# Kernel optimization log

Measured on AMD Instinct MI355X. Metric: run time of the kernel, lower is better.

## Reference

```python
import jax, jax.numpy as jnp
import numpy as np

N = 16384        # tokens (batch*seq)
D_MODEL = 4096
D_HALF = D_MODEL // 2
NUM_EXPERTS = 64
TOP_K = 4
SCALE = 2.0


def setup_inputs() -> dict:
    key = jax.random.key(0)
    k_u, k_ex, k_ey = jax.random.split(key, 3)
    u = jax.random.normal(k_u, (N, D_MODEL), dtype=jnp.float32)
    E_x = jax.random.normal(k_ex, (D_HALF, NUM_EXPERTS), dtype=jnp.float32) * 0.01
    E_y = jax.random.normal(k_ey, (D_HALF, NUM_EXPERTS), dtype=jnp.float32) * 0.01
    bias = jnp.zeros((NUM_EXPERTS,), dtype=jnp.float32)
    # torus-shape scalar parameters (torch init values)
    c = jnp.float32(2.0)
    d = jnp.float32(2.0)
    a1 = jnp.float32(4.0)
    b1 = jnp.float32(4.0)
    return {"u": u, "E_x": E_x, "E_y": E_y, "bias": bias,
            "c": c, "d": d, "a1": a1, "b1": b1, "top_k": TOP_K}


def reference(u, E_x, E_y, bias, c, d, a1, b1, top_k):
    d_half = E_x.shape[0]
    num_experts = E_x.shape[1]
    # dual small GEMM + tanh squash onto [-scale, scale]
    x = jnp.tanh(u[..., :d_half] @ E_x) * SCALE        # [N, E]
    y = jnp.tanh(u[..., d_half:] @ E_y) * SCALE        # [N, E]
    xa, ya = jnp.abs(x), jnp.abs(y)
    # 4CM torus: f(x,y) = (|x|^a1 + |y|^b1) * exp(-(|x|^c + |y|^d))
    scores = (xa ** a1 + ya ** b1) * jnp.exp(-(xa ** c + ya ** d)) + bias
    topk_s, topk_i = jax.lax.top_k(scores, top_k)       # [N, k]
    probs = jax.nn.softmax(scores, axis=-1)             # [N, E]
    aux_loss = jnp.sum(jnp.mean(probs, axis=0) ** 2) * num_experts
    return topk_i, topk_s, scores, aux_loss
```

## Files before the change

### kernel.cpp

```cpp
#include <hip/hip_runtime.h>
#include <math.h>

#define N_TOK 16384
#define DM    4096
#define DH    2048
#define NE    64
#define TBK   64
#define TOPK  4
#define KQ    1024
#define NSTEP 32

#define OFF_TI  0
#define OFF_TS  (N_TOK * TOPK)
#define OFF_SC  (N_TOK * TOPK * 2)
#define OFF_AUX (N_TOK * TOPK * 2 + N_TOK * NE)

typedef __attribute__((ext_vector_type(4)))  float  f32x4;
typedef __attribute__((ext_vector_type(16))) float  f32x16;
typedef __attribute__((ext_vector_type(8)))  __bf16 bf16x8;

#define BSPLIT_ELEMS (2 * 64 * 3 * 2 * 2 * 64 * 8)

__device__ __forceinline__ void split3(float a, __bf16& h, __bf16& m, __bf16& l) {
    h = (__bf16)a;
    float r = a - (float)h;
    m = (__bf16)r;
    float r2 = r - (float)m;
    l = (__bf16)r2;
}

__global__ __launch_bounds__(256) void prep_B(
    const float* __restrict__ Ex, const float* __restrict__ Ey,
    __bf16* __restrict__ Bws)
{
    const int t    = blockIdx.x * 256 + threadIdx.x;
    const int lane = t & 63;
    const int sk   = (t >> 6) & 1;
    const int et   = (t >> 7) & 1;
    const int ks   = (t >> 8) & 63;
    const int h    = (t >> 14) & 1;
    const float* E = h ? Ey : Ex;
    const int e  = et * 32 + (lane & 31);
    const int k0 = ks * 32 + sk * 16 + (lane >> 5) * 8;
    bf16x8 vh, vm, vl;
    #pragma unroll
    for (int j = 0; j < 8; ++j) {
        __bf16 hh, mm, ll;
        split3(E[(size_t)(k0 + j) * NE + e], hh, mm, ll);
        vh[j] = hh; vm[j] = mm; vl[j] = ll;
    }
    #pragma unroll
    for (int s = 0; s < 3; ++s) {
        size_t base = ((((((size_t)h * 64 + ks) * 3 + s) * 2 + et) * 2 + sk) * 64 + lane) * 8;
        *(bf16x8*)(Bws + base) = (s == 0) ? vh : (s == 1) ? vm : vl;
    }
}

__global__ __launch_bounds__(512, 2) void torus_mfma(
    const float* __restrict__ u, const __bf16* __restrict__ Bws,
    const float* __restrict__ bias,
    const float* __restrict__ cp, const float* __restrict__ dp,
    const float* __restrict__ a1p, const float* __restrict__ b1p,
    float* __restrict__ out, float* __restrict__ esum)
{
    __shared__ float pre[2][NE][68];
    __shared__ float stile[TBK][NE + 1];
    __shared__ float s_m[TBK], s_inv[TBK];

    const int tid  = threadIdx.x;
    const int t0   = blockIdx.x * TBK;
    const int lane = tid & 63;
    const int wv   = tid >> 6;
    const int h    = wv >> 2;
    const int kh   = (wv >> 1) & 1;
    const int th   = wv & 1;
    const int lr   = lane & 31;
    const int lkh  = lane >> 5;

    const float* ap = u + (size_t)(t0 + th * 32 + lr) * DM + h * DH + kh * KQ + lkh * 8;
    const __bf16* bp0 = Bws + ((size_t)h * 64 + kh * 32) * 6144 + lane * 8;

    f32x16 acc[2] = {};
    f32x4  rA[2][4];

    auto load_raw = [&](f32x4 (&r)[4], int s) {
        const float* p = ap + s * 32;
        r[0] = *(const f32x4*)(p);
        r[1] = *(const f32x4*)(p + 4);
        r[2] = *(const f32x4*)(p + 16);
        r[3] = *(const f32x4*)(p + 20);
    };

    auto step = [&](int s, f32x4 (&r)[4]) {
        const __bf16* bp = bp0 + (size_t)s * 6144;
        bf16x8 bh[2][2], bm[2][2], bl[2][2];
        #pragma unroll
        for (int et = 0; et < 2; ++et)
            #pragma unroll
            for (int sk = 0; sk < 2; ++sk) {
                bh[et][sk] = *(const bf16x8*)(bp + (0 * 4 + et * 2 + sk) * 512);
                bm[et][sk] = *(const bf16x8*)(bp + (1 * 4 + et * 2 + sk) * 512);
                bl[et][sk] = *(const bf16x8*)(bp + (2 * 4 + et * 2 + sk) * 512);
            }
        bf16x8 sh[2], sm[2], sl[2];
        #pragma unroll
        for (int sk = 0; sk < 2; ++sk)
            #pragma unroll
            for (int q = 0; q < 2; ++q)
                #pragma unroll
                for (int j = 0; j < 4; ++j) {
                    __bf16 hh, mm, ll;
                    split3(r[sk * 2 + q][j], hh, mm, ll);
                    sh[sk][q * 4 + j] = hh; sm[sk][q * 4 + j] = mm; sl[sk][q * 4 + j] = ll;
                }
        const int sp = (s + 2 < NSTEP) ? s + 2 : s;
        load_raw(r, sp);
        #pragma unroll
        for (int et = 0; et < 2; ++et)
            #pragma unroll
            for (int sk = 0; sk < 2; ++sk) {
                acc[et] = __builtin_amdgcn_mfma_f32_32x32x16_bf16(sh[sk], bh[et][sk], acc[et], 0, 0, 0);
                acc[et] = __builtin_amdgcn_mfma_f32_32x32x16_bf16(sm[sk], bh[et][sk], acc[et], 0, 0, 0);
                acc[et] = __builtin_amdgcn_mfma_f32_32x32x16_bf16(sl[sk], bh[et][sk], acc[et], 0, 0, 0);
            }
        #pragma unroll
        for (int et = 0; et < 2; ++et)
            #pragma unroll
            for (int sk = 0; sk < 2; ++sk) {
                acc[et] = __builtin_amdgcn_mfma_f32_32x32x16_bf16(sh[sk], bm[et][sk], acc[et], 0, 0, 0);
                acc[et] = __builtin_amdgcn_mfma_f32_32x32x16_bf16(sm[sk], bm[et][sk], acc[et], 0, 0, 0);
            }
        #pragma unroll
        for (int et = 0; et < 2; ++et)
            #pragma unroll
            for (int sk = 0; sk < 2; ++sk)
                acc[et] = __builtin_amdgcn_mfma_f32_32x32x16_bf16(sh[sk], bl[et][sk], acc[et], 0, 0, 0);
    };

    load_raw(rA[0], 0);
    load_raw(rA[1], 1);
    #pragma unroll 1
    for (int s = 0; s < NSTEP; s += 2) {
        step(s,     rA[0]);
        step(s + 1, rA[1]);
    }

    __syncthreads();
    if (kh == 0) {
        #pragma unroll
        for (int et = 0; et < 2; ++et)
            #pragma unroll
            for (int q = 0; q < 4; ++q) {
                int e  = et * 32 + lr;
                int tk = th * 32 + q * 8 + 4 * lkh;
                f32x4 v = { acc[et][q*4+0], acc[et][q*4+1], acc[et][q*4+2], acc[et][q*4+3] };
                *(f32x4*)&pre[h][e][tk] = v;
            }
    }
    __syncthreads();
    if (kh == 1) {
        #pragma unroll
        for (int et = 0; et < 2; ++et)
            #pragma unroll
            for (int q = 0; q < 4; ++q) {
                int e  = et * 32 + lr;
                int tk = th * 32 + q * 8 + 4 * lkh;
                f32x4 v = { acc[et][q*4+0], acc[et][q*4+1], acc[et][q*4+2], acc[et][q*4+3] };
                f32x4 o = *(f32x4*)&pre[h][e][tk];
                v += o;
                *(f32x4*)&pre[h][e][tk] = v;
            }
    }
    __syncthreads();

    {
        const float c_ = *cp, d_ = *dp, a1_ = *a1p, b1_ = *b1p;
        const int tk = tid & 63;
        const int e0 = (tid >> 6) * 8;
        #pragma unroll
        for (int i = 0; i < 8; ++i) {
            int e = e0 + i;
            float x = pre[0][e][tk];
            float y = pre[1][e][tk];
            x = tanhf(x) * 2.0f; y = tanhf(y) * 2.0f;
            float xa = fabsf(x), ya = fabsf(y);
            float sc = (powf(xa, a1_) + powf(ya, b1_)) *
                       expf(-(powf(xa, c_) + powf(ya, d_))) + bias[e];
            stile[tk][e] = sc;
        }
    }
    __syncthreads();

    if (tid < TBK) {
        const int t = tid;
        float bv[TOPK]; int bi[TOPK];
        #pragma unroll
        for (int p = 0; p < TOPK; ++p) {
            float best = -INFINITY; int besti = 0;
            for (int e = 0; e < NE; ++e) {
                float v = stile[t][e];
                bool taken = false;
                #pragma unroll
                for (int q = 0; q < p; ++q) taken = taken || (bi[q] == e);
                if (!taken && v > best) { best = v; besti = e; }
            }
            bv[p] = best; bi[p] = besti;
        }
        const float m = bv[0];
        float denom = 0.0f;
        for (int e = 0; e < NE; ++e) denom += expf(stile[t][e] - m);
        const float inv = 1.0f / denom;
        s_m[t] = m; s_inv[t] = inv;
        #pragma unroll
        for (int p = 0; p < TOPK; ++p) {
            out[OFF_TI + (size_t)(t0 + t) * TOPK + p] = (float)bi[p];
            out[OFF_TS + (size_t)(t0 + t) * TOPK + p] = bv[p];
        }
    }
    __syncthreads();

    if (tid < NE) {
        const int e = tid;
        float cs = 0.0f;
        for (int t = 0; t < TBK; ++t)
            cs += expf(stile[t][e] - s_m[t]) * s_inv[t];
        atomicAdd(&esum[e], cs);
    }

    for (int idx = tid; idx < TBK * NE; idx += 512)
        out[OFF_SC + (size_t)t0 * NE + idx] = stile[idx >> 6][idx & (NE - 1)];
}

__global__ __launch_bounds__(64) void torus_aux(const float* __restrict__ esum,
                                                float* __restrict__ out)
{
    const int e = threadIdx.x;
    float s = esum[e] * (1.0f / (float)N_TOK);
    float v = s * s;
    #pragma unroll
    for (int off = 32; off > 0; off >>= 1) v += __shfl_down(v, off);
    if (e == 0) out[OFF_AUX] = v * (float)NE;
}

extern "C" void kernel_launch(void* const* d_in, const int* in_sizes, int n_in,
                              void* d_out, int out_size, void* d_ws, size_t ws_size,
                              hipStream_t stream) {
    const float* u    = (const float*)d_in[0];
    const float* Ex   = (const float*)d_in[1];
    const float* Ey   = (const float*)d_in[2];
    const float* bias = (const float*)d_in[3];
    const float* cp   = (const float*)d_in[4];
    const float* dp   = (const float*)d_in[5];
    const float* a1p  = (const float*)d_in[6];
    const float* b1p  = (const float*)d_in[7];
    float* out = (float*)d_out;
    __bf16* Bws = (__bf16*)d_ws;
    float* esum = (float*)((char*)d_ws + (size_t)BSPLIT_ELEMS * sizeof(__bf16));

    prep_B<<<128, 256, 0, stream>>>(Ex, Ey, Bws);
    hipMemsetAsync(esum, 0, NE * sizeof(float), stream);
    torus_mfma<<<N_TOK / TBK, 512, 0, stream>>>(u, Bws, bias, cp, dp, a1p, b1p, out, esum);
    torus_aux<<<1, 64, 0, stream>>>(esum, out);
}
```

Baseline: 131.8 us.

## Split fused router into GEMM kernel and separate epilogue kernel with smaller tiles

Result: slower. 260.7 us (+97.7%).

```diff
diff --git a/kernel.cpp b/kernel.cpp
--- a/kernel.cpp
+++ b/kernel.cpp
@@ -1,13 +1,14 @@
 #include <hip/hip_runtime.h>
 #include <math.h>
+#include <stdint.h>
 
 #define N_TOK 16384
 #define DM    4096
 #define DH    2048
 #define NE    64
-#define TBK   64
+#define TBG   32
+#define TBE   64
 #define TOPK  4
-#define KQ    1024
 #define NSTEP 32
 
 #define OFF_TI  0
@@ -18,8 +19,10 @@
 typedef __attribute__((ext_vector_type(4)))  float  f32x4;
 typedef __attribute__((ext_vector_type(16))) float  f32x16;
 typedef __attribute__((ext_vector_type(8)))  __bf16 bf16x8;
+typedef __attribute__((ext_vector_type(8)))  unsigned short u16x8;
 
 #define BSPLIT_ELEMS (2 * 64 * 3 * 2 * 2 * 64 * 8)
+#define PRE_BYTE_OFF (2u * 1024u * 1024u)
 
 __device__ __forceinline__ void split3(float a, __bf16& h, __bf16& m, __bf16& l) {
     h = (__bf16)a;
@@ -56,34 +59,30 @@
     }
 }
 
-__global__ __launch_bounds__(512, 2) void torus_mfma(
+__global__ __launch_bounds__(256, 4) void gemm_partial(
     const float* __restrict__ u, const __bf16* __restrict__ Bws,
-    const float* __restrict__ bias,
-    const float* __restrict__ cp, const float* __restrict__ dp,
-    const float* __restrict__ a1p, const float* __restrict__ b1p,
-    float* __restrict__ out, float* __restrict__ esum)
-{
-    __shared__ float pre[2][NE][68];
-    __shared__ float stile[TBK][NE + 1];
-    __shared__ float s_m[TBK], s_inv[TBK];
+    float* __restrict__ pre)
+{
+    __shared__ float part[2][TBG][36];
 
     const int tid  = threadIdx.x;
-    const int t0   = blockIdx.x * TBK;
+    const int tile = blockIdx.x >> 1;
+    const int h    = blockIdx.x & 1;
+    const int t0   = tile * TBG;
     const int lane = tid & 63;
     const int wv   = tid >> 6;
-    const int h    = wv >> 2;
-    const int kh   = (wv >> 1) & 1;
-    const int th   = wv & 1;
+    const int et   = wv & 1;
+    const int kd   = wv >> 1;
     const int lr   = lane & 31;
     const int lkh  = lane >> 5;
 
-    const float* ap = u + (size_t)(t0 + th * 32 + lr) * DM + h * DH + kh * KQ + lkh * 8;
-    const __bf16* bp0 = Bws + ((size_t)h * 64 + kh * 32) * 6144 + lane * 8;
+    const float*  ap  = u + (size_t)(t0 + lr) * DM + h * DH + kd * 1024 + lkh * 8;
+    const __bf16* bp0 = Bws + (size_t)(h * 64 + kd * 32) * 6144 + et * 1024 + lane * 8;
 
     f32x16 acc[2] = {};
     f32x4  rA[2][4];
 
-    auto load_raw = [&](f32x4 (&r)[4], int s) {
+    auto loadA = [&](f32x4 (&r)[4], int s) {
         const float* p = ap + s * 32;
         r[0] = *(const f32x4*)(p);
         r[1] = *(const f32x4*)(p + 4);
@@ -91,107 +90,132 @@
         r[3] = *(const f32x4*)(p + 20);
     };
 
-    auto step = [&](int s, f32x4 (&r)[4]) {
+    auto body = [&](int s, f32x4 (&r)[4]) {
         const __bf16* bp = bp0 + (size_t)s * 6144;
-        bf16x8 bh[2][2], bm[2][2], bl[2][2];
-        #pragma unroll
-        for (int et = 0; et < 2; ++et)
-            #pragma unroll
-            for (int sk = 0; sk < 2; ++sk) {
-                bh[et][sk] = *(const bf16x8*)(bp + (0 * 4 + et * 2 + sk) * 512);
-                bm[et][sk] = *(const bf16x8*)(bp + (1 * 4 + et * 2 + sk) * 512);
-                bl[et][sk] = *(const bf16x8*)(bp + (2 * 4 + et * 2 + sk) * 512);
-            }
-        bf16x8 sh[2], sm[2], sl[2];
+        bf16x8 bh0 = *(const bf16x8*)(bp);
+        bf16x8 bh1 = *(const bf16x8*)(bp + 512);
+        bf16x8 bm0 = *(const bf16x8*)(bp + 2048);
+        bf16x8 bm1 = *(const bf16x8*)(bp + 2560);
+        bf16x8 bl0 = *(const bf16x8*)(bp + 4096);
+        bf16x8 bl1 = *(const bf16x8*)(bp + 4608);
+        __builtin_amdgcn_sched_barrier(0);
+        u16x8 sh[2], sm[2], sl[2];
         #pragma unroll
         for (int sk = 0; sk < 2; ++sk)
             #pragma unroll
             for (int q = 0; q < 2; ++q)
                 #pragma unroll
                 for (int j = 0; j < 4; ++j) {
-                    __bf16 hh, mm, ll;
-                    split3(r[sk * 2 + q][j], hh, mm, ll);
-                    sh[sk][q * 4 + j] = hh; sm[sk][q * 4 + j] = mm; sl[sk][q * 4 + j] = ll;
+                    float a = r[sk * 2 + q][j];
+                    unsigned h32 = __float_as_uint(a) & 0xFFFF0000u;
+                    float rr = a - __uint_as_float(h32);
+                    unsigned m32 = __float_as_uint(rr) & 0xFFFF0000u;
+                    float r2f = rr - __uint_as_float(m32);
+                    sh[sk][q * 4 + j] = (unsigned short)(h32 >> 16);
+                    sm[sk][q * 4 + j] = (unsigned short)(m32 >> 16);
+                    sl[sk][q * 4 + j] = (unsigned short)(__float_as_uint(r2f) >> 16);
                 }
         const int sp = (s + 2 < NSTEP) ? s + 2 : s;
-        load_raw(r, sp);
-        #pragma unroll
-        for (int et = 0; et < 2; ++et)
-            #pragma unroll
-            for (int sk = 0; sk < 2; ++sk) {
-                acc[et] = __builtin_amdgcn_mfma_f32_32x32x16_bf16(sh[sk], bh[et][sk], acc[et], 0, 0, 0);
-                acc[et] = __builtin_amdgcn_mfma_f32_32x32x16_bf16(sm[sk], bh[et][sk], acc[et], 0, 0, 0);
-                acc[et] = __builtin_amdgcn_mfma_f32_32x32x16_bf16(sl[sk], bh[et][sk], acc[et], 0, 0, 0);
-            }
-        #pragma unroll
-        for (int et = 0; et < 2; ++et)
-            #pragma unroll
-            for (int sk = 0; sk < 2; ++sk) {
-                acc[et] = __builtin_amdgcn_mfma_f32_32x32x16_bf16(sh[sk], bm[et][sk], acc[et], 0, 0, 0);
-                acc[et] = __builtin_amdgcn_mfma_f32_32x32x16_bf16(sm[sk], bm[et][sk], acc[et], 0, 0, 0);
-            }
-        #pragma unroll
-        for (int et = 0; et < 2; ++et)
-            #pragma unroll
-            for (int sk = 0; sk < 2; ++sk)
-                acc[et] = __builtin_amdgcn_mfma_f32_32x32x16_bf16(sh[sk], bl[et][sk], acc[et], 0, 0, 0);
+        loadA(r, sp);
+        __builtin_amdgcn_sched_barrier(0);
+        {
+            bf16x8 vh_ = __builtin_bit_cast(bf16x8, sh[0]);
+            bf16x8 vm_ = __builtin_bit_cast(bf16x8, sm[0]);
+            bf16x8 vl_ = __builtin_bit_cast(bf16x8, sl[0]);
+            acc[0] = __builtin_amdgcn_mfma_f32_32x32x16_bf16(vh_, bh0, acc[0], 0, 0, 0);
+            acc[0] = __builtin_amdgcn_mfma_f32_32x32x16_bf16(vm_, bh0, acc[0], 0, 0, 0);
+            acc[0] = __builtin_amdgcn_mfma_f32_32x32x16_bf16(vl_, bh0, acc[0], 0, 0, 0);
+            acc[0] = __builtin_amdgcn_mfma_f32_32x32x16_bf16(vh_, bm0, acc[0], 0, 0, 0);
+            acc[0] = __builtin_amdgcn_mfma_f32_32x32x16_bf16(vm_, bm0, acc[0], 0, 0, 0);
+            acc[0] = __builtin_amdgcn_mfma_f32_32x32x16_bf16(vh_, bl0, acc[0], 0, 0, 0);
+        }
+        {
+            bf16x8 vh_ = __builtin_bit_cast(bf16x8, sh[1]);
+            bf16x8 vm_ = __builtin_bit_cast(bf16x8, sm[1]);
+            bf16x8 vl_ = __builtin_bit_cast(bf16x8, sl[1]);
+            acc[1] = __builtin_amdgcn_mfma_f32_32x32x16_bf16(vh_, bh1, acc[1], 0, 0, 0);
+            acc[1] = __builtin_amdgcn_mfma_f32_32x32x16_bf16(vm_, bh1, acc[1], 0, 0, 0);
+            acc[1] = __builtin_amdgcn_mfma_f32_32x32x16_bf16(vl_, bh1, acc[1], 0, 0, 0);
+            acc[1] = __builtin_amdgcn_mfma_f32_32x32x16_bf16(vh_, bm1, acc[1], 0, 0, 0);
+            acc[1] = __builtin_amdgcn_mfma_f32_32x32x16_bf16(vm_, bm1, acc[1], 0, 0, 0);
+            acc[1] = __builtin_amdgcn_mfma_f32_32x32x16_bf16(vh_, bl1, acc[1], 0, 0, 0);
+        }
+        __builtin_amdgcn_sched_barrier(0);
     };
 
-    load_raw(rA[0], 0);
-    load_raw(rA[1], 1);
+    loadA(rA[0], 0);
+    loadA(rA[1], 1);
     #pragma unroll 1
     for (int s = 0; s < NSTEP; s += 2) {
-        step(s,     rA[0]);
-        step(s + 1, rA[1]);
-    }
-
-    __syncthreads();
-    if (kh == 0) {
-        #pragma unroll
-        for (int et = 0; et < 2; ++et)
-            #pragma unroll
-            for (int q = 0; q < 4; ++q) {
-                int e  = et * 32 + lr;
-                int tk = th * 32 + q * 8 + 4 * lkh;
-                f32x4 v = { acc[et][q*4+0], acc[et][q*4+1], acc[et][q*4+2], acc[et][q*4+3] };
-                *(f32x4*)&pre[h][e][tk] = v;
-            }
-    }
-    __syncthreads();
-    if (kh == 1) {
-        #pragma unroll
-        for (int et = 0; et < 2; ++et)
-            #pragma unroll
-            for (int q = 0; q < 4; ++q) {
-                int e  = et * 32 + lr;
-                int tk = th * 32 + q * 8 + 4 * lkh;
-                f32x4 v = { acc[et][q*4+0], acc[et][q*4+1], acc[et][q*4+2], acc[et][q*4+3] };
-                f32x4 o = *(f32x4*)&pre[h][e][tk];
-                v += o;
-                *(f32x4*)&pre[h][e][tk] = v;
-            }
-    }
-    __syncthreads();
+        body(s,     rA[0]);
+        body(s + 1, rA[1]);
+    }
+
+    f32x16 a = acc[0] + acc[1];
+    __syncthreads();
+    if (kd == 0) {
+        #pragma unroll
+        for (int q = 0; q < 4; ++q)
+            #pragma unroll
+            for (int j = 0; j < 4; ++j)
+                part[et][j + 8 * q + 4 * lkh][lr] = a[q * 4 + j];
+    }
+    __syncthreads();
+    if (kd == 1) {
+        #pragma unroll
+        for (int q = 0; q < 4; ++q)
+            #pragma unroll
+            for (int j = 0; j < 4; ++j)
+                part[et][j + 8 * q + 4 * lkh][lr] += a[q * 4 + j];
+    }
+    __syncthreads();
+    {
+        const int tok = tid >> 3;
+        const int e0  = (tid & 7) * 8;
+        float* dst = pre + ((size_t)h * N_TOK + t0 + tok) * NE + e0;
+        const float* src = &part[e0 >> 5][tok][e0 & 31];
+        *(f32x4*)(dst)     = *(const f32x4*)(src);
+        *(f32x4*)(dst + 4) = *(const f32x4*)(src + 4);
+    }
+}
+
+__global__ __launch_bounds__(256) void torus_ep(
+    const float* __restrict__ pre, const float* __restrict__ bias,
+    const float* __restrict__ cp, const float* __restrict__ dp,
+    const float* __restrict__ a1p, const float* __restrict__ b1p,
+    float* __restrict__ out, float* __restrict__ esum)
+{
+    __shared__ float stile[TBE][NE + 1];
+    __shared__ float s_m[TBE], s_inv[TBE];
+
+    const int tid = threadIdx.x;
+    const int t0  = blockIdx.x * TBE;
 
     {
         const float c_ = *cp, d_ = *dp, a1_ = *a1p, b1_ = *b1p;
-        const int tk = tid & 63;
-        const int e0 = (tid >> 6) * 8;
-        #pragma unroll
-        for (int i = 0; i < 8; ++i) {
-            int e = e0 + i;
-            float x = pre[0][e][tk];
-            float y = pre[1][e][tk];
-            x = tanhf(x) * 2.0f; y = tanhf(y) * 2.0f;
-            float xa = fabsf(x), ya = fabsf(y);
-            float sc = (powf(xa, a1_) + powf(ya, b1_)) *
-                       expf(-(powf(xa, c_) + powf(ya, d_))) + bias[e];
-            stile[tk][e] = sc;
-        }
-    }
-    __syncthreads();
-
-    if (tid < TBK) {
+        const int tok = tid >> 2;
+        const int e0  = (tid & 3) * 16;
+        const float* px = pre + (size_t)(t0 + tok) * NE + e0;
+        const float* py = pre + ((size_t)N_TOK + t0 + tok) * NE + e0;
+        #pragma unroll
+        for (int i = 0; i < 16; i += 4) {
+            f32x4 xv = *(const f32x4*)(px + i);
+            f32x4 yv = *(const f32x4*)(py + i);
+            #pragma unroll
+            for (int j = 0; j < 4; ++j) {
+                int e = e0 + i + j;
+                float x = tanhf(xv[j]) * 2.0f;
+                float y = tanhf(yv[j]) * 2.0f;
+                float xa = fabsf(x), ya = fabsf(y);
+                float sc = (powf(xa, a1_) + powf(ya, b1_)) *
+                           expf(-(powf(xa, c_) + powf(ya, d_))) + bias[e];
+                stile[tok][e] = sc;
+            }
+        }
+    }
+    __syncthreads();
+
+    if (tid < TBE) {
         const int t = tid;
         float bv[TOPK]; int bi[TOPK];
         #pragma unroll
@@ -222,12 +246,12 @@
     if (tid < NE) {
         const int e = tid;
         float cs = 0.0f;
-        for (int t = 0; t < TBK; ++t)
+        for (int t = 0; t < TBE; ++t)
             cs += expf(stile[t][e] - s_m[t]) * s_inv[t];
         atomicAdd(&esum[e], cs);
     }
 
-    for (int idx = tid; idx < TBK * NE; idx += 512)
+    for (int idx = tid; idx < TBE * NE; idx += 256)
         out[OFF_SC + (size_t)t0 * NE + idx] = stile[idx >> 6][idx & (NE - 1)];
 }
 
@@ -253,12 +277,14 @@
     const float* dp   = (const float*)d_in[5];
     const float* a1p  = (const float*)d_in[6];
     const float* b1p  = (const float*)d_in[7];
-    float* out = (float*)d_out;
+    float* out  = (float*)d_out;
     __bf16* Bws = (__bf16*)d_ws;
     float* esum = (float*)((char*)d_ws + (size_t)BSPLIT_ELEMS * sizeof(__bf16));
+    float* pre  = (float*)((char*)d_ws + PRE_BYTE_OFF);
 
     prep_B<<<128, 256, 0, stream>>>(Ex, Ey, Bws);
     hipMemsetAsync(esum, 0, NE * sizeof(float), stream);
-    torus_mfma<<<N_TOK / TBK, 512, 0, stream>>>(u, Bws, bias, cp, dp, a1p, b1p, out, esum);
+    gemm_partial<<<N_TOK / TBG * 2, 256, 0, stream>>>(u, Bws, pre);
+    torus_ep<<<N_TOK / TBE, 256, 0, stream>>>(pre, bias, cp, dp, a1p, b1p, out, esum);
     torus_aux<<<1, 64, 0, stream>>>(esum, out);
 }
```
